# Kernel tuning notes

Hardware: AMD Instinct MI355X
Metric: run time of the kernel (lower is better)

## Reference

```python
import jax, jax.numpy as jnp
import numpy as np

N, N_BINS = 100000, 512
BATCH, K = 8192, 16


def setup_inputs() -> dict:
    key = jax.random.key(0)
    k1, k2, k3 = jax.random.split(key, 3)
    outputs = jax.random.uniform(k1, (N, N_BINS), dtype=jnp.float32)
    # y holds (float-encoded) neighbor indices; trunc(y) must index rows of outputs
    y = jax.random.randint(k2, (BATCH, K), 0, N).astype(jnp.float32)
    weights = jax.random.uniform(k3, (BATCH,), dtype=jnp.float32)
    return {"outputs": outputs, "y": y, "weights": weights}


def reference(outputs, y, weights):
    n, n_bins = outputs.shape
    batch_size, k = y.shape
    nns = jnp.trunc(y).astype(jnp.int32)  # (B, k) indices into outputs rows

    # Torch builds add[a,b,c] = outputs[nns[c,a], b] + outputs[c, b] with shape
    # (k, n_bins, batch) then maxes over bins. Equivalent, batch-major layout:
    o_nn = outputs[nns]  # (B, k, n_bins) gather
    add = jnp.max(o_nn + outputs[:batch_size, None, :], axis=-1)  # (B, k)

    booster_weights = jnp.clip((2.0 - jnp.mean(add, axis=1)) / 2.0, 0.5)  # (B,)
    add_mean = jnp.mean(add * weights[:, None])
    diff = jnp.square(2.0 - add_mean)

    target_b = n / n_bins
    b_col = jnp.sum(outputs[:batch_size], axis=0)  # (n_bins,)
    b = jnp.max(b_col) - jnp.min(b_col)

    cost = b / target_b + diff
    return (cost, diff, b / target_b, booster_weights)
```

## Files before the change

kernel.cpp:

```cpp
#include <hip/hip_runtime.h>

#define NBINS 512

__global__ void init_ws_kernel(float* __restrict__ ws, int n) {
    int t = blockIdx.x * blockDim.x + threadIdx.x;
    if (t < n) ws[t] = 0.0f;
}

__global__ __launch_bounds__(256) void main_kernel(
        const float* __restrict__ outputs,
        const float* __restrict__ y,
        const float* __restrict__ weights,
        float* __restrict__ out,
        float* __restrict__ accum,
        int K) {
    __shared__ float s_add[16];

    const int b = blockIdx.x;
    const int t = threadIdx.x;
    const int w = t >> 6;
    const int lane = t & 63;

    const float4 yv = ((const float4*)(y + (size_t)b * K))[w];
    const int nn0 = (int)yv.x;
    const int nn1 = (int)yv.y;
    const int nn2 = (int)yv.z;
    const int nn3 = (int)yv.w;

    const float4* bp = (const float4*)(outputs + (size_t)b * NBINS);
    const float4* r0 = (const float4*)(outputs + (size_t)nn0 * NBINS);
    const float4* r1 = (const float4*)(outputs + (size_t)nn1 * NBINS);
    const float4* r2 = (const float4*)(outputs + (size_t)nn2 * NBINS);
    const float4* r3 = (const float4*)(outputs + (size_t)nn3 * NBINS);

    const int i0 = lane * 2;
    const int i1 = lane * 2 + 1;

    float4 base0 = bp[i0], base1 = bp[i1];
    float4 a0 = r0[i0], a1 = r0[i1];
    float4 c0 = r1[i0], c1 = r1[i1];
    float4 d0 = r2[i0], d1 = r2[i1];
    float4 e0 = r3[i0], e1 = r3[i1];

    float m0 = fmaxf(fmaxf(fmaxf(a0.x + base0.x, a0.y + base0.y),
                           fmaxf(a0.z + base0.z, a0.w + base0.w)),
                     fmaxf(fmaxf(a1.x + base1.x, a1.y + base1.y),
                           fmaxf(a1.z + base1.z, a1.w + base1.w)));
    float m1 = fmaxf(fmaxf(fmaxf(c0.x + base0.x, c0.y + base0.y),
                           fmaxf(c0.z + base0.z, c0.w + base0.w)),
                     fmaxf(fmaxf(c1.x + base1.x, c1.y + base1.y),
                           fmaxf(c1.z + base1.z, c1.w + base1.w)));
    float m2 = fmaxf(fmaxf(fmaxf(d0.x + base0.x, d0.y + base0.y),
                           fmaxf(d0.z + base0.z, d0.w + base0.w)),
                     fmaxf(fmaxf(d1.x + base1.x, d1.y + base1.y),
                           fmaxf(d1.z + base1.z, d1.w + base1.w)));
    float m3 = fmaxf(fmaxf(fmaxf(e0.x + base0.x, e0.y + base0.y),
                           fmaxf(e0.z + base0.z, e0.w + base0.w)),
                     fmaxf(fmaxf(e1.x + base1.x, e1.y + base1.y),
                           fmaxf(e1.z + base1.z, e1.w + base1.w)));

    #pragma unroll
    for (int off = 32; off > 0; off >>= 1) {
        m0 = fmaxf(m0, __shfl_down(m0, off, 64));
        m1 = fmaxf(m1, __shfl_down(m1, off, 64));
        m2 = fmaxf(m2, __shfl_down(m2, off, 64));
        m3 = fmaxf(m3, __shfl_down(m3, off, 64));
    }

    if (lane == 0) {
        s_add[w * 4 + 0] = m0;
        s_add[w * 4 + 1] = m1;
        s_add[w * 4 + 2] = m2;
        s_add[w * 4 + 3] = m3;
    }
    __syncthreads();

    if (t == 0) {
        float sum = 0.0f;
        #pragma unroll
        for (int i = 0; i < 16; ++i) sum += s_add[i];
        float mean = sum * (1.0f / 16.0f);
        float booster = fmaxf(0.5f, (2.0f - mean) * 0.5f);
        out[3 + b] = booster;
        atomicAdd(&accum[b & 255], weights[b] * sum);
    }
}

__global__ void colsum_kernel(const float* __restrict__ outputs,
                              float* __restrict__ bcol,
                              int rows_per_block) {
    const int t = threadIdx.x;
    const int r0 = blockIdx.x * rows_per_block;
    float local = 0.0f;
    for (int r = 0; r < rows_per_block; ++r)
        local += outputs[(size_t)(r0 + r) * NBINS + t];
    atomicAdd(&bcol[t], local);
}

__global__ void final_kernel(const float* __restrict__ bcol,
                             const float* __restrict__ accum,
                             float* __restrict__ out,
                             float inv_count, float inv_target) {
    __shared__ float smax[NBINS];
    __shared__ float smin[NBINS];
    const int t = threadIdx.x;
    float v = bcol[t];
    smax[t] = v;
    smin[t] = v;
    __syncthreads();
    for (int s = NBINS / 2; s > 0; s >>= 1) {
        if (t < s) {
            smax[t] = fmaxf(smax[t], smax[t + s]);
            smin[t] = fminf(smin[t], smin[t + s]);
        }
        __syncthreads();
    }
    if (t == 0) {
        float acc = 0.0f;
        for (int i = 0; i < 256; ++i) acc += accum[i];
        float add_mean = acc * inv_count;
        float d = 2.0f - add_mean;
        float diff = d * d;
        float bn = (smax[0] - smin[0]) * inv_target;
        out[0] = bn + diff;
        out[1] = diff;
        out[2] = bn;
    }
}

extern "C" void kernel_launch(void* const* d_in, const int* in_sizes, int n_in,
                              void* d_out, int out_size, void* d_ws, size_t ws_size,
                              hipStream_t stream) {
    const float* outputs = (const float*)d_in[0];
    const float* y       = (const float*)d_in[1];
    const float* weights = (const float*)d_in[2];
    float* out = (float*)d_out;

    const int B = in_sizes[2];
    const int K = in_sizes[1] / B;
    const int N = in_sizes[0] / NBINS;

    float* ws    = (float*)d_ws;
    float* bcol  = ws;
    float* accum = ws + NBINS;

    init_ws_kernel<<<1, 1024, 0, stream>>>(ws, NBINS + 256);

    main_kernel<<<B, (K / 4) * 64, 0, stream>>>(outputs, y, weights, out, accum, K);

    const int rows_per_block = 32;
    colsum_kernel<<<B / rows_per_block, NBINS, 0, stream>>>(outputs, bcol, rows_per_block);

    final_kernel<<<1, NBINS, 0, stream>>>(bcol, accum, out,
                                          1.0f / (float)(B * K),
                                          (float)NBINS / (float)N);
}
```

Before: 299.2 us.

## Fuse column-sum into main kernel and replace atomics with partial buffers

Merges the column-sum work into the main gather kernel as extra blocks. The init kernel and separate colsum launch go away, which cuts two launches. Atomic accumulation is replaced by per-block partial results in the workspace, and the final kernel reduces those deterministically. The cost is a larger workspace and more serial reading in the single-block final kernel (256×512 partials plus B sums).

```diff
diff --git a/kernel.cpp b/kernel.cpp
--- a/kernel.cpp
+++ b/kernel.cpp
@@ -1,23 +1,36 @@
 #include <hip/hip_runtime.h>
 
 #define NBINS 512
+#define COL_BLOCKS 256
 
-__global__ void init_ws_kernel(float* __restrict__ ws, int n) {
-    int t = blockIdx.x * blockDim.x + threadIdx.x;
-    if (t < n) ws[t] = 0.0f;
-}
-
-__global__ __launch_bounds__(256) void main_kernel(
+__global__ __launch_bounds__(256) void fused_kernel(
         const float* __restrict__ outputs,
         const float* __restrict__ y,
         const float* __restrict__ weights,
         float* __restrict__ out,
-        float* __restrict__ accum,
-        int K) {
+        float* __restrict__ ws,
+        int B, int K) {
+    const int t = threadIdx.x;
+
+    if ((int)blockIdx.x >= B) {
+        const int c = blockIdx.x - B;
+        const int rows = B / COL_BLOCKS;
+        const float* base = outputs + (size_t)c * rows * NBINS;
+        float l0 = 0.0f, l1 = 0.0f;
+        #pragma unroll 4
+        for (int r = 0; r < rows; ++r) {
+            l0 += base[(size_t)r * NBINS + t];
+            l1 += base[(size_t)r * NBINS + t + 256];
+        }
+        float* dst = ws + B + (size_t)c * NBINS;
+        dst[t] = l0;
+        dst[t + 256] = l1;
+        return;
+    }
+
     __shared__ float s_add[16];
 
     const int b = blockIdx.x;
-    const int t = threadIdx.x;
     const int w = t >> 6;
     const int lane = t & 63;
 
@@ -82,43 +95,44 @@
         float mean = sum * (1.0f / 16.0f);
         float booster = fmaxf(0.5f, (2.0f - mean) * 0.5f);
         out[3 + b] = booster;
-        atomicAdd(&accum[b & 255], weights[b] * sum);
+        ws[b] = weights[b] * sum;
     }
 }
 
-__global__ void colsum_kernel(const float* __restrict__ outputs,
-                              float* __restrict__ bcol,
-                              int rows_per_block) {
-    const int t = threadIdx.x;
-    const int r0 = blockIdx.x * rows_per_block;
-    float local = 0.0f;
-    for (int r = 0; r < rows_per_block; ++r)
-        local += outputs[(size_t)(r0 + r) * NBINS + t];
-    atomicAdd(&bcol[t], local);
-}
-
-__global__ void final_kernel(const float* __restrict__ bcol,
-                             const float* __restrict__ accum,
-                             float* __restrict__ out,
-                             float inv_count, float inv_target) {
+__global__ __launch_bounds__(512) void final_kernel(
+        const float* __restrict__ ws,
+        float* __restrict__ out,
+        int B, float inv_count, float inv_target) {
+    __shared__ float ssum[NBINS];
     __shared__ float smax[NBINS];
     __shared__ float smin[NBINS];
     const int t = threadIdx.x;
-    float v = bcol[t];
-    smax[t] = v;
-    smin[t] = v;
+
+    float acc = 0.0f;
+    #pragma unroll 4
+    for (int j = t; j < B; j += NBINS)
+        acc += ws[j];
+    ssum[t] = acc;
+
+    const float* part = ws + B;
+    float colv = 0.0f;
+    #pragma unroll 8
+    for (int c = 0; c < COL_BLOCKS; ++c)
+        colv += part[(size_t)c * NBINS + t];
+    smax[t] = colv;
+    smin[t] = colv;
     __syncthreads();
+
     for (int s = NBINS / 2; s > 0; s >>= 1) {
         if (t < s) {
+            ssum[t] += ssum[t + s];
             smax[t] = fmaxf(smax[t], smax[t + s]);
             smin[t] = fminf(smin[t], smin[t + s]);
         }
         __syncthreads();
     }
     if (t == 0) {
-        float acc = 0.0f;
-        for (int i = 0; i < 256; ++i) acc += accum[i];
-        float add_mean = acc * inv_count;
+        float add_mean = ssum[0] * inv_count;
         float d = 2.0f - add_mean;
         float diff = d * d;
         float bn = (smax[0] - smin[0]) * inv_target;
@@ -140,18 +154,11 @@
     const int K = in_sizes[1] / B;
     const int N = in_sizes[0] / NBINS;
 
-    float* ws    = (float*)d_ws;
-    float* bcol  = ws;
-    float* accum = ws + NBINS;
+    float* ws = (float*)d_ws;
 
-    init_ws_kernel<<<1, 1024, 0, stream>>>(ws, NBINS + 256);
+    fused_kernel<<<B + COL_BLOCKS, 256, 0, stream>>>(outputs, y, weights, out, ws, B, K);
 
-    main_kernel<<<B, (K / 4) * 64, 0, stream>>>(outputs, y, weights, out, accum, K);
-
-    const int rows_per_block = 32;
-    colsum_kernel<<<B / rows_per_block, NBINS, 0, stream>>>(outputs, bcol, rows_per_block);
-
-    final_kernel<<<1, NBINS, 0, stream>>>(bcol, accum, out,
+    final_kernel<<<1, NBINS, 0, stream>>>(ws, out, B,
                                           1.0f / (float)(B * K),
                                           (float)NBINS / (float)N);
 }
```

Result: faster. 290.9 us (-2.8%).
